# Optimization experiments

Measured on AMD Instinct MI355X. Metric: run time of the kernel, lower is better.

## Reference

```python
import jax, jax.numpy as jnp
import numpy as np
from functools import partial

N, C, D, H, W = 2, 64, 8, 96, 96
G, K, PAD = 2, 3, 1
P = K ** 3
CG = C // G
AXIS_SCALE = jnp.array([0.5, 1.0, 1.0], dtype=jnp.float32)  # applied to (dx, dy, dz)
OFFSET_SCALE = 1.0  # converged warmup scale
EPS = 1e-5


def setup_inputs() -> dict:
    key = jax.random.key(0)
    ks = jax.random.split(key, 13)
    s = 0.05
    return {
        "x": jax.random.normal(ks[0], (N, C, D, H, W), jnp.float32),
        "w_pre": jax.random.normal(ks[1], (C, C), jnp.float32) * s,
        "w_in": jax.random.normal(ks[2], (C, C), jnp.float32) * s,
        "b_in": jnp.zeros((C,), jnp.float32),
        "w_dw": jax.random.normal(ks[3], (C, 1, K, K, K), jnp.float32) * s,
        "w_off": jax.random.normal(ks[4], (C, G * P * 3), jnp.float32) * s,
        "b_off": jnp.zeros((G * P * 3,), jnp.float32),
        "w_mask": jax.random.normal(ks[5], (C, G * P), jnp.float32) * s,
        "b_mask": jnp.zeros((G * P,), jnp.float32),
        "w_out": jax.random.normal(ks[6], (C, C), jnp.float32) * s,
        "b_out": jnp.zeros((C,), jnp.float32),
        "w_post": jax.random.normal(ks[7], (C, C), jnp.float32) * s,
        "gate": jnp.zeros((), jnp.float32),
    }


def _instance_norm(x):  # x: [N, C, D, H, W], normalize over spatial dims per (n, c)
    mean = jnp.mean(x, axis=(2, 3, 4), keepdims=True)
    var = jnp.var(x, axis=(2, 3, 4), keepdims=True)
    return (x - mean) * jax.lax.rsqrt(var + EPS)


def _dcn_core(x_proj, offset, mask):
    # x_proj: [N, D, H, W, C]; offset: [N, D, H, W, G, P, 3] (dx, dy, dz); mask: [N, D, H, W, G, P]
    Dp, Hp, Wp = D + 2 * PAD, H + 2 * PAD, W + 2 * PAD
    x_pad = jnp.pad(x_proj, ((0, 0), (PAD, PAD), (PAD, PAD), (PAD, PAD), (0, 0)))
    x_pad = x_pad.reshape(N, Dp, Hp, Wp, G, CG)

    n_idx = jnp.arange(N).reshape(N, 1, 1, 1, 1)
    g_idx = jnp.arange(G).reshape(1, 1, 1, 1, G)
    zg = jnp.arange(D, dtype=jnp.float32).reshape(1, D, 1, 1, 1)
    yg = jnp.arange(H, dtype=jnp.float32).reshape(1, 1, H, 1, 1)
    xg = jnp.arange(W, dtype=jnp.float32).reshape(1, 1, 1, W, 1)

    def trilinear(zs, ys, xs):  # each [N, D, H, W, G] float coords in padded frame
        z0 = jnp.floor(zs); y0 = jnp.floor(ys); x0 = jnp.floor(xs)
        fz = zs - z0; fy = ys - y0; fx = xs - x0
        z0i = z0.astype(jnp.int32); y0i = y0.astype(jnp.int32); x0i = x0.astype(jnp.int32)
        res = None
        for dz in (0, 1):
            wz = fz if dz else 1.0 - fz
            zi = z0i + dz
            for dy in (0, 1):
                wy = fy if dy else 1.0 - fy
                yi = y0i + dy
                for dx in (0, 1):
                    wx = fx if dx else 1.0 - fx
                    xi = x0i + dx
                    valid = ((zi >= 0) & (zi < Dp) & (yi >= 0) & (yi < Hp)
                             & (xi >= 0) & (xi < Wp)).astype(zs.dtype)
                    g = x_pad[n_idx, jnp.clip(zi, 0, Dp - 1), jnp.clip(yi, 0, Hp - 1),
                              jnp.clip(xi, 0, Wp - 1), g_idx]  # [N,D,H,W,G,CG]
                    term = g * (wz * wy * wx * valid)[..., None]
                    res = term if res is None else res + term
        return res

    # kernel grid points (z-major), base position in padded frame is out_idx + k_idx
    kk = jnp.arange(K, dtype=jnp.float32)
    kz, ky, kx = jnp.meshgrid(kk, kk, kk, indexing="ij")
    kpts = jnp.stack([kz.ravel(), ky.ravel(), kx.ravel()], axis=-1)  # [P, 3]

    off = offset * (AXIS_SCALE * OFFSET_SCALE)  # scale (dx, dy, dz)
    off_p = jnp.moveaxis(off, 5, 0)    # [P, N, D, H, W, G, 3]
    mask_p = jnp.moveaxis(mask, 5, 0)  # [P, N, D, H, W, G]

    def body(acc, inp):
        o, m, kp = inp
        zs = zg + kp[0] + o[..., 2]
        ys = yg + kp[1] + o[..., 1]
        xs = xg + kp[2] + o[..., 0]
        samp = trilinear(zs, ys, xs)  # [N,D,H,W,G,CG]
        return acc + m[..., None] * samp, None

    acc0 = jnp.zeros((N, D, H, W, G, CG), x_proj.dtype)
    acc, _ = jax.lax.scan(body, acc0, (off_p, mask_p, kpts))
    return acc.reshape(N, D, H, W, C)


def _forward(x, w_pre, w_in, b_in, w_dw, w_off, b_off, w_mask, b_mask, w_out, b_out, w_post, gate):
    pre = jnp.einsum("ncdhw,oc->nodhw", x, w_pre)  # 1x1x1 conv, no bias
    x_cl = jnp.transpose(pre, (0, 2, 3, 4, 1))     # [N,D,H,W,C]
    x_proj = x_cl @ w_in + b_in
    # depthwise 3x3x3 conv + InstanceNorm + GELU for the offset/mask branch
    dw = jax.lax.conv_general_dilated(
        pre, w_dw, window_strides=(1, 1, 1), padding=((PAD, PAD),) * 3,
        feature_group_count=C, dimension_numbers=("NCDHW", "OIDHW", "NCDHW"))
    dw = jax.nn.gelu(_instance_norm(dw))
    feat = jnp.transpose(dw, (0, 2, 3, 4, 1))      # [N,D,H,W,C]
    offset = (feat @ w_off + b_off).reshape(N, D, H, W, G, P, 3)
    mask = jax.nn.softmax((feat @ w_mask + b_mask).reshape(N, D, H, W, G, P), axis=-1)
    core = _dcn_core(x_proj, offset, mask)         # [N,D,H,W,C]
    out = core @ w_out + b_out
    y = jnp.transpose(out, (0, 4, 1, 2, 3))        # back to NCDHW
    y = jnp.einsum("ncdhw,oc->nodhw", y, w_post)   # post 1x1x1 conv
    return x + jax.nn.sigmoid(gate) * y


def reference(x, w_pre, w_in, b_in, w_dw, w_off, b_off, w_mask, b_mask, w_out, b_out, w_post, gate):
    return _forward(x, w_pre, w_in, b_in, w_dw, w_off, b_off, w_mask, b_mask, w_out, b_out, w_post, gate)
```

## Files before the change

### kernel.cpp

```cpp
#include <hip/hip_runtime.h>
#include <math.h>

#define N_ 2
#define C_ 64
#define D_ 8
#define H_ 96
#define W_ 96
#define S_ (D_*H_*W_)
#define HW_ (H_*W_)
#define ZP_ 12
#define YP_ 100
#define XP_ 100
#define NSTR_ (ZP_*YP_*XP_*64)
#define ZS_ (YP_*XP_*64)
#define YS_ (XP_*64)

__device__ __forceinline__ float gelu_fast(float x) {
    float a = 0.7978845608028654f * (x + 0.044715f*x*x*x);
    float E = __expf(2.f*a);
    return x - x * __builtin_amdgcn_rcpf(E + 1.f);
}

__device__ __forceinline__ unsigned short f2bf(float f) {
    unsigned u = __float_as_uint(f);
    unsigned r = (u + 0x7fffu + ((u >> 16) & 1u)) >> 16;
    return (unsigned short)r;
}

__global__ __launch_bounds__(64) void k_prep(const float* __restrict__ w_out,
        const float* __restrict__ b_out, const float* __restrict__ w_post,
        const float* __restrict__ w_off, const float* __restrict__ b_off,
        const float* __restrict__ w_mask, const float* __restrict__ b_mask,
        float* __restrict__ W2, float* __restrict__ B2,
        float4* __restrict__ woffT4, float4* __restrict__ b4f) {
    int b = blockIdx.x;
    int t = threadIdx.x;
    float acc = 0.f;
    for (int c = 0; c < 64; ++c)
        acc = fmaf(w_out[b*64+c], w_post[t*64+c], acc);
    W2[b*64 + t] = acc;
    if (b == 0) {
        float a2 = 0.f;
        for (int c = 0; c < 64; ++c)
            a2 = fmaf(w_post[t*64+c], b_out[c], a2);
        B2[t] = a2;
    }
    if (t < 54) {
        int c = b, u = t;
        woffT4[c*64 + u] = make_float4(w_off[c*162 + u*3] * 0.5f,
                                       w_off[c*162 + u*3 + 1],
                                       w_off[c*162 + u*3 + 2],
                                       w_mask[c*54 + u]);
        if (b == 1)
            b4f[u] = make_float4(b_off[u*3] * 0.5f, b_off[u*3+1], b_off[u*3+2],
                                 b_mask[u]);
    }
}

__global__ __launch_bounds__(256) void k_pre_proj(const float* __restrict__ x,
        const float* __restrict__ w_pre, const float* __restrict__ w_in,
        const float* __restrict__ b_in, float* __restrict__ pre,
        unsigned short* __restrict__ xprojP) {
    __shared__ float lx[64][65];
    __shared__ float lwa[64][65];
    __shared__ float lwb[64][65];
    int b = blockIdx.x;
    int n = b / 1152;
    int s0 = (b % 1152) * 64;
    int tid = threadIdx.x;
    for (int idx = tid; idx < 1024; idx += 256) {
        int r = idx >> 4, q4 = (idx & 15) * 4;
        float4 vx = *(const float4*)&x[((size_t)(n*C_ + r))*S_ + s0 + q4];
        lx[r][q4] = vx.x; lx[r][q4+1] = vx.y; lx[r][q4+2] = vx.z; lx[r][q4+3] = vx.w;
        float4 va = *(const float4*)&w_pre[r*64 + q4];
        lwa[r][q4] = va.x; lwa[r][q4+1] = va.y; lwa[r][q4+2] = va.z; lwa[r][q4+3] = va.w;
        float4 vb = *(const float4*)&w_in[r*64 + q4];
        lwb[r][q4] = vb.x; lwb[r][q4+1] = vb.y; lwb[r][q4+2] = vb.z; lwb[r][q4+3] = vb.w;
    }
    __syncthreads();
    int o0 = (tid & 15) * 4;
    int v0 = (tid >> 4) * 4;
    float acc[4][4] = {};
    #pragma unroll 8
    for (int c = 0; c < 64; ++c) {
        float xv[4], wv[4];
        #pragma unroll
        for (int j = 0; j < 4; ++j) { xv[j] = lx[c][v0+j]; wv[j] = lwa[o0+j][c]; }
        #pragma unroll
        for (int vj = 0; vj < 4; ++vj)
            #pragma unroll
            for (int oj = 0; oj < 4; ++oj)
                acc[vj][oj] = fmaf(xv[vj], wv[oj], acc[vj][oj]);
    }
    #pragma unroll
    for (int vj = 0; vj < 4; ++vj) {
        float4 r = make_float4(acc[vj][0], acc[vj][1], acc[vj][2], acc[vj][3]);
        *(float4*)&pre[((size_t)(n*S_ + s0 + v0 + vj))*64 + o0] = r;
    }
    __syncthreads();
    #pragma unroll
    for (int vj = 0; vj < 4; ++vj)
        #pragma unroll
        for (int oj = 0; oj < 4; ++oj)
            lx[v0+vj][o0+oj] = acc[vj][oj];
    __syncthreads();
    float acc2[4][4];
    #pragma unroll
    for (int oj = 0; oj < 4; ++oj) {
        float bo = b_in[o0+oj];
        #pragma unroll
        for (int vj = 0; vj < 4; ++vj) acc2[vj][oj] = bo;
    }
    #pragma unroll 8
    for (int c = 0; c < 64; ++c) {
        float fv[4], wv[4];
        #pragma unroll
        for (int j = 0; j < 4; ++j) { fv[j] = lx[v0+j][c]; wv[j] = lwb[c][o0+j]; }
        #pragma unroll
        for (int vj = 0; vj < 4; ++vj)
            #pragma unroll
            for (int oj = 0; oj < 4; ++oj)
                acc2[vj][oj] = fmaf(fv[vj], wv[oj], acc2[vj][oj]);
    }
    #pragma unroll
    for (int vj = 0; vj < 4; ++vj) {
        int vox = s0 + v0 + vj;
        int z = vox / HW_;
        int rem = vox - z*HW_;
        int y = rem / W_;
        int xq = rem - y*W_;
        size_t pw = (size_t)n*NSTR_ + (size_t)(z+2)*ZS_ + (y+2)*YS_ + (xq+2)*64 + o0;
        ushort4 pk;
        pk.x = f2bf(acc2[vj][0]); pk.y = f2bf(acc2[vj][1]);
        pk.z = f2bf(acc2[vj][2]); pk.w = f2bf(acc2[vj][3]);
        *(ushort4*)&xprojP[pw] = pk;
    }
}

__global__ __launch_bounds__(256) void k_dw_stats(const float* __restrict__ pre,
        const float* __restrict__ w_dw, float* __restrict__ dw,
        float* __restrict__ psum, float* __restrict__ pss) {
    __shared__ float4 lwd[27][16];
    __shared__ float4 lsum[16][16];
    __shared__ float4 lssum[16][16];
    int b = blockIdx.x;
    int y = b % H_;
    int z = (b / H_) % D_;
    int n = b / (D_*H_);
    int tid = threadIdx.x;
    if (tid < 27*16) {
        int k = tid >> 4, c4 = tid & 15;
        lwd[k][c4] = make_float4(w_dw[(c4*4+0)*27 + k], w_dw[(c4*4+1)*27 + k],
                                 w_dw[(c4*4+2)*27 + k], w_dw[(c4*4+3)*27 + k]);
    }
    __syncthreads();
    int c4 = tid & 15, xg = tid >> 4;
    const float* preN = pre + (size_t)n*S_*64;
    float4 s4 = make_float4(0,0,0,0), ss4 = make_float4(0,0,0,0);
    for (int xx = 0; xx < 6; ++xx) {
        int xi = xg + xx*16;
        float4 acc = make_float4(0,0,0,0);
        #pragma unroll
        for (int dz = 0; dz < 3; ++dz) {
            int zz = z + dz - 1;
            if (zz < 0 || zz >= D_) continue;
            #pragma unroll
            for (int dy = 0; dy < 3; ++dy) {
                int yy = y + dy - 1;
                if (yy < 0 || yy >= H_) continue;
                int rowb = (zz*HW_ + yy*W_)*64 + c4*4;
                #pragma unroll
                for (int dx = 0; dx < 3; ++dx) {
                    int xn = xi + dx - 1;
                    if ((unsigned)xn < (unsigned)W_) {
                        float4 v = *(const float4*)&preN[rowb + (xn<<6)];
                        float4 w = lwd[dz*9+dy*3+dx][c4];
                        acc.x = fmaf(v.x, w.x, acc.x);
                        acc.y = fmaf(v.y, w.y, acc.y);
                        acc.z = fmaf(v.z, w.z, acc.z);
                        acc.w = fmaf(v.w, w.w, acc.w);
                    }
                }
            }
        }
        *(float4*)&dw[((size_t)n*S_ + z*HW_ + y*W_ + xi)*64 + c4*4] = acc;
        s4.x += acc.x; s4.y += acc.y; s4.z += acc.z; s4.w += acc.w;
        ss4.x = fmaf(acc.x, acc.x, ss4.x); ss4.y = fmaf(acc.y, acc.y, ss4.y);
        ss4.z = fmaf(acc.z, acc.z, ss4.z); ss4.w = fmaf(acc.w, acc.w, ss4.w);
    }
    lsum[xg][c4] = s4; lssum[xg][c4] = ss4;
    __syncthreads();
    if (tid < 64) {
        float s = 0.f, ss = 0.f;
        #pragma unroll
        for (int k = 0; k < 16; ++k) {
            s  += ((const float*)&lsum [k][tid>>2])[tid&3];
            ss += ((const float*)&lssum[k][tid>>2])[tid&3];
        }
        psum[tid*1536 + b] = s;
        pss [tid*1536 + b] = ss;
    }
}

__global__ void k_stats2(const float* __restrict__ psum, const float* __restrict__ pss,
                         float* __restrict__ stats) {
    int u = blockIdx.x;
    int n = u >> 6, c = u & 63;
    int l = threadIdx.x;
    float s = 0.f, ss = 0.f;
    #pragma unroll
    for (int k = 0; k < 12; ++k) {
        int row = n*768 + k*64 + l;
        s  += psum[c*1536 + row];
        ss += pss [c*1536 + row];
    }
    #pragma unroll
    for (int o2 = 32; o2 >= 1; o2 >>= 1) {
        s  += __shfl_xor(s, o2);
        ss += __shfl_xor(ss, o2);
    }
    if (l == 0) {
        float inv = 1.f / (float)S_;
        float mean = s * inv;
        float var = ss * inv - mean*mean;
        stats[n*128 + c] = mean;
        stats[n*128 + 64 + c] = rsqrtf(var + 1e-5f);
    }
}

__global__ __launch_bounds__(256) void k_dcn(const unsigned short* __restrict__ xprojP,
        const float* __restrict__ dw, const float* __restrict__ stats,
        const float4* __restrict__ woffT4, const float4* __restrict__ b4f,
        float* __restrict__ core) {
    __shared__ float featT[64][36];
    __shared__ float4 offs4[64][29];
    int tid = threadIdx.x;
    int orig = blockIdx.x;
    int bid = (orig & 7) * 576 + (orig >> 3);
    int x8 = bid % 12;
    int t1 = bid / 12;
    int y4 = t1 % 24;
    int t2 = t1 / 24;
    int z  = t2 & 7;
    int n  = t2 >> 3;
    int yb = y4*4, xb = x8*8;
    size_t voxBase = (size_t)n*S_ + (size_t)z*HW_ + yb*W_ + xb;

    {
        int c4 = (tid & 15) * 4;
        int vp = tid >> 4;
        #pragma unroll
        for (int j = 0; j < 2; ++j) {
            int vloc = vp*2 + j;
            size_t vox = voxBase + (vloc>>3)*W_ + (vloc & 7);
            float4 v = *(const float4*)&dw[vox*64 + c4];
            float vals[4] = {v.x, v.y, v.z, v.w};
            #pragma unroll
            for (int jj = 0; jj < 4; ++jj) {
                int c = c4 + jj;
                float t = (vals[jj] - stats[n*128+c]) * stats[n*128+64+c];
                featT[c][vloc] = gelu_fast(t);
            }
        }
    }
    __syncthreads();

    if (tid < 216) {
        int q = tid / 54;
        int u = tid - q*54;
        int g = u / 27, p = u - g*27;
        float4 bb = b4f[u];
        float4 aa[8];
        #pragma unroll
        for (int j = 0; j < 8; ++j) aa[j] = bb;
        for (int c = 0; c < 64; ++c) {
            float4 w = woffT4[c*64 + u];
            float4 f0 = *(const float4*)&featT[c][q*8];
            float4 f1 = *(const float4*)&featT[c][q*8 + 4];
            float ff[8] = {f0.x, f0.y, f0.z, f0.w, f1.x, f1.y, f1.z, f1.w};
            #pragma unroll
            for (int j = 0; j < 8; ++j) {
                aa[j].x = fmaf(ff[j], w.x, aa[j].x);
                aa[j].y = fmaf(ff[j], w.y, aa[j].y);
                aa[j].z = fmaf(ff[j], w.z, aa[j].z);
                aa[j].w = fmaf(ff[j], w.w, aa[j].w);
            }
        }
        #pragma unroll
        for (int j = 0; j < 8; ++j)
            offs4[(q*8+j)*2 + g][p] = aa[j];
    }
    __syncthreads();

    if (tid < 64) {
        float mx = -1e30f;
        #pragma unroll
        for (int p = 0; p < 27; ++p) mx = fmaxf(mx, offs4[tid][p].w);
        float e[27]; float ssum = 0.f;
        #pragma unroll
        for (int p = 0; p < 27; ++p) { e[p] = __expf(offs4[tid][p].w - mx); ssum += e[p]; }
        float inv = __builtin_amdgcn_rcpf(ssum);
        #pragma unroll
        for (int p = 0; p < 27; ++p) offs4[tid][p].w = e[p]*inv;
    }
    __syncthreads();

    int pair = tid >> 2;
    int vloc = pair >> 1, g = pair & 1;
    int yy = vloc >> 3, xx = vloc & 7;
    int yv = yb + yy, xv = xb + xx;
    int ch4 = (tid & 3) * 8;
    const unsigned short* __restrict__ base = xprojP + (size_t)n*NSTR_;
    int Kc = 2*ZS_ + 2*YS_ + 128 + g*32 + ch4;
    float fzb = (float)(z-1), fyb = (float)(yv-1), fxb = (float)(xv-1);
    float a0=0.f,a1=0.f,a2=0.f,a3=0.f,a4=0.f,a5=0.f,a6=0.f,a7=0.f;
    #pragma unroll
    for (int p = 0; p < 27; ++p) {
        float4 tp = offs4[pair][p];
        float zf = fzb + (float)(p/9) + tp.z;
        float yf = fyb + (float)((p/3)%3) + tp.y;
        float xf = fxb + (float)(p%3) + tp.x;
        zf = fminf(fmaxf(zf, -1.5f), (float)D_ + 0.5f);
        yf = fminf(fmaxf(yf, -1.5f), (float)H_ + 0.5f);
        xf = fminf(fmaxf(xf, -1.5f), (float)W_ + 0.5f);
        float z0f = floorf(zf), y0f = floorf(yf), x0f = floorf(xf);
        float fz = zf - z0f, fy = yf - y0f, fx = xf - x0f;
        int zi = (int)z0f, yi = (int)y0f, xi = (int)x0f;
        float wz1 = fz * tp.w, wz0 = tp.w - wz1;
        float wy1 = fy, wy0 = 1.f - fy;
        float wx1 = fx, wx0 = 1.f - fx;
        float w00 = wz0*wy0, w01 = wz0*wy1, w10 = wz1*wy0, w11 = wz1*wy1;
        float c000 = w00*wx0, c001 = w00*wx1, c010 = w01*wx0, c011 = w01*wx1;
        float c100 = w10*wx0, c101 = w10*wx1, c110 = w11*wx0, c111 = w11*wx1;
        int cw = zi*ZS_ + yi*YS_ + (xi << 6) + Kc;
        const unsigned short* p00 = base + cw;
        const unsigned short* p01 = p00 + YS_;
        const unsigned short* p10 = p00 + ZS_;
        const unsigned short* p11 = p10 + YS_;
        uint4 q000 = *(const uint4*)p00;
        uint4 q001 = *(const uint4*)(p00 + 64);
        uint4 q010 = *(const uint4*)p01;
        uint4 q011 = *(const uint4*)(p01 + 64);
        uint4 q100 = *(const uint4*)p10;
        uint4 q101 = *(const uint4*)(p10 + 64);
        uint4 q110 = *(const uint4*)p11;
        uint4 q111 = *(const uint4*)(p11 + 64);
        #define ACC8(Q, WGT) { \
            float wq = (WGT); \
            a0 = fmaf(wq, __uint_as_float((Q).x << 16), a0); \
            a1 = fmaf(wq, __uint_as_float((Q).x & 0xffff0000u), a1); \
            a2 = fmaf(wq, __uint_as_float((Q).y << 16), a2); \
            a3 = fmaf(wq, __uint_as_float((Q).y & 0xffff0000u), a3); \
            a4 = fmaf(wq, __uint_as_float((Q).z << 16), a4); \
            a5 = fmaf(wq, __uint_as_float((Q).z & 0xffff0000u), a5); \
            a6 = fmaf(wq, __uint_as_float((Q).w << 16), a6); \
            a7 = fmaf(wq, __uint_as_float((Q).w & 0xffff0000u), a7); \
        }
        ACC8(q000, c000); ACC8(q001, c001); ACC8(q010, c010); ACC8(q011, c011);
        ACC8(q100, c100); ACC8(q101, c101); ACC8(q110, c110); ACC8(q111, c111);
        #undef ACC8
    }
    size_t voxOut = voxBase + yy*W_ + xx;
    size_t ob = voxOut*64 + g*32 + ch4;
    *(float4*)&core[ob]     = make_float4(a0, a1, a2, a3);
    *(float4*)&core[ob + 4] = make_float4(a4, a5, a6, a7);
}

__global__ __launch_bounds__(256) void k_final(const float* __restrict__ core,
        const float* __restrict__ W2, const float* __restrict__ B2,
        const float* __restrict__ x, const float* __restrict__ gate,
        float* __restrict__ out) {
    __shared__ float lc[64][65];
    __shared__ float lw[64][65];
    int b = blockIdx.x;
    int n = b / 1152;
    int s0 = (b % 1152) * 64;
    int tid = threadIdx.x;
    for (int idx = tid; idx < 1024; idx += 256) {
        int r = idx >> 4, q4 = (idx & 15) * 4;
        float4 vc = *(const float4*)&core[((size_t)(n*S_ + s0 + r))*64 + q4];
        lc[r][q4] = vc.x; lc[r][q4+1] = vc.y; lc[r][q4+2] = vc.z; lc[r][q4+3] = vc.w;
        float4 vw = *(const float4*)&W2[r*64 + q4];
        lw[r][q4] = vw.x; lw[r][q4+1] = vw.y; lw[r][q4+2] = vw.z; lw[r][q4+3] = vw.w;
    }
    __syncthreads();
    float sg = 1.f / (1.f + expf(-gate[0]));
    int o0 = (tid & 15) * 4;
    int v0 = (tid >> 4) * 4;
    float acc[4][4];
    #pragma unroll
    for (int oj = 0; oj < 4; ++oj) {
        float bo = B2[o0+oj];
        #pragma unroll
        for (int vj = 0; vj < 4; ++vj) acc[vj][oj] = bo;
    }
    #pragma unroll 8
    for (int c = 0; c < 64; ++c) {
        float fv[4], wv[4];
        #pragma unroll
        for (int j = 0; j < 4; ++j) { fv[j] = lc[v0+j][c]; wv[j] = lw[c][o0+j]; }
        #pragma unroll
        for (int vj = 0; vj < 4; ++vj)
            #pragma unroll
            for (int oj = 0; oj < 4; ++oj)
                acc[vj][oj] = fmaf(fv[vj], wv[oj], acc[vj][oj]);
    }
    #pragma unroll
    for (int oj = 0; oj < 4; ++oj) {
        size_t gi = ((size_t)(n*64 + o0 + oj))*S_ + s0 + v0;
        float4 xv = *(const float4*)&x[gi];
        float4 r;
        r.x = fmaf(sg, acc[0][oj], xv.x);
        r.y = fmaf(sg, acc[1][oj], xv.y);
        r.z = fmaf(sg, acc[2][oj], xv.z);
        r.w = fmaf(sg, acc[3][oj], xv.w);
        *(float4*)&out[gi] = r;
    }
}

extern "C" void kernel_launch(void* const* d_in, const int* in_sizes, int n_in,
                              void* d_out, int out_size, void* d_ws, size_t ws_size,
                              hipStream_t stream) {
    const float* x      = (const float*)d_in[0];
    const float* w_pre  = (const float*)d_in[1];
    const float* w_in   = (const float*)d_in[2];
    const float* b_in   = (const float*)d_in[3];
    const float* w_dw   = (const float*)d_in[4];
    const float* w_off  = (const float*)d_in[5];
    const float* b_off  = (const float*)d_in[6];
    const float* w_mask = (const float*)d_in[7];
    const float* b_mask = (const float*)d_in[8];
    const float* w_out  = (const float*)d_in[9];
    const float* b_out  = (const float*)d_in[10];
    const float* w_post = (const float*)d_in[11];
    const float* gate   = (const float*)d_in[12];
    float* out = (float*)d_out;

    float* ws      = (float*)d_ws;
    unsigned short* xprojP = (unsigned short*)ws;
    float* preCore = ws + (size_t)7680000;
    float* psum    = preCore + (size_t)9437184;
    float* pss     = psum + 98304;
    float* stats   = pss + 98304;
    float* W2      = stats + 256;
    float* B2      = W2 + 4096;
    float4* woffT4 = (float4*)(B2 + 128);
    float4* b4f    = woffT4 + 4096;
    float* dwb     = out;

    hipMemsetAsync(xprojP, 0, (size_t)15360000*sizeof(unsigned short), stream);
    hipLaunchKernelGGL(k_prep,     dim3(64),   dim3(64),  0, stream,
                       w_out, b_out, w_post, w_off, b_off, w_mask, b_mask,
                       W2, B2, woffT4, b4f);
    hipLaunchKernelGGL(k_pre_proj, dim3(2304), dim3(256), 0, stream,
                       x, w_pre, w_in, b_in, preCore, xprojP);
    hipLaunchKernelGGL(k_dw_stats, dim3(1536), dim3(256), 0, stream,
                       preCore, w_dw, dwb, psum, pss);
    hipLaunchKernelGGL(k_stats2,   dim3(128),  dim3(64),  0, stream, psum, pss, stats);
    hipLaunchKernelGGL(k_dcn,      dim3(4608), dim3(256), 0, stream,
                       xprojP, dwb, stats, woffT4, b4f, preCore);
    hipLaunchKernelGGL(k_final,    dim3(2304), dim3(256), 0, stream,
                       preCore, W2, B2, x, gate, out);
}
```

Measured before the change: 340.8 us.

## Precompute DCN sampling coords once per block and store core output as bf16

Bilinear corner weights and gather base offsets are now computed once per (voxel, group, point) in a cooperative shared-memory pass, instead of being recomputed by each of the four channel-slice threads. The weights are packed as bf16 pairs and the offsets are stored in a shared union that reuses the feature buffer. The DCN output tensor is written as bf16 rather than fp32, halving the intermediate write and the read in the final kernel. Costs are an extra barrier, bf16 rounding of the interpolation weights and the core values, and a small error from reading the high bf16 half without masking off the low bits.

Result: faster. 329.4 us (-3.3%).

```diff
diff --git a/kernel.cpp b/kernel.cpp
--- a/kernel.cpp
+++ b/kernel.cpp
@@ -25,6 +25,10 @@
     unsigned u = __float_as_uint(f);
     unsigned r = (u + 0x7fffu + ((u >> 16) & 1u)) >> 16;
     return (unsigned short)r;
+}
+
+__device__ __forceinline__ unsigned pkhi(float a, float b) {
+    return __builtin_amdgcn_perm(__float_as_uint(a), __float_as_uint(b), 0x07060302u);
 }
 
 __global__ __launch_bounds__(64) void k_prep(const float* __restrict__ w_out,
@@ -231,8 +235,11 @@
 __global__ __launch_bounds__(256) void k_dcn(const unsigned short* __restrict__ xprojP,
         const float* __restrict__ dw, const float* __restrict__ stats,
         const float4* __restrict__ woffT4, const float4* __restrict__ b4f,
-        float* __restrict__ core) {
-    __shared__ float featT[64][36];
+        unsigned short* __restrict__ coreB) {
+    __shared__ union {
+        float featT[64][36];
+        int   cwl[64][27];
+    } uS;
     __shared__ float4 offs4[64][29];
     int tid = threadIdx.x;
     int orig = blockIdx.x;
@@ -259,7 +266,7 @@
             for (int jj = 0; jj < 4; ++jj) {
                 int c = c4 + jj;
                 float t = (vals[jj] - stats[n*128+c]) * stats[n*128+64+c];
-                featT[c][vloc] = gelu_fast(t);
+                uS.featT[c][vloc] = gelu_fast(t);
             }
         }
     }
@@ -275,8 +282,8 @@
         for (int j = 0; j < 8; ++j) aa[j] = bb;
         for (int c = 0; c < 64; ++c) {
             float4 w = woffT4[c*64 + u];
-            float4 f0 = *(const float4*)&featT[c][q*8];
-            float4 f1 = *(const float4*)&featT[c][q*8 + 4];
+            float4 f0 = *(const float4*)&uS.featT[c][q*8];
+            float4 f1 = *(const float4*)&uS.featT[c][q*8 + 4];
             float ff[8] = {f0.x, f0.y, f0.z, f0.w, f1.x, f1.y, f1.z, f1.w};
             #pragma unroll
             for (int j = 0; j < 8; ++j) {
@@ -305,34 +312,52 @@
     }
     __syncthreads();
 
+    {
+        int zm1 = z - 1;
+        #pragma unroll
+        for (int k = 0; k < 7; ++k) {
+            int idx = tid + k*256;
+            if (idx < 1728) {
+                int pair = idx / 27;
+                int p = idx - pair*27;
+                float4 tp = offs4[pair][p];
+                int vloc = pair >> 1, g = pair & 1;
+                int yy = vloc >> 3, xx = vloc & 7;
+                float zf = (float)(zm1 + p/9) + tp.z;
+                float yf = (float)(yb + yy - 1 + (p/3)%3) + tp.y;
+                float xf = (float)(xb + xx - 1 + p%3) + tp.x;
+                zf = fminf(fmaxf(zf, -1.5f), (float)D_ + 0.5f);
+                yf = fminf(fmaxf(yf, -1.5f), (float)H_ + 0.5f);
+                xf = fminf(fmaxf(xf, -1.5f), (float)W_ + 0.5f);
+                float z0f = floorf(zf), y0f = floorf(yf), x0f = floorf(xf);
+                float fz = zf - z0f, fy = yf - y0f, fx = xf - x0f;
+                int zi = (int)z0f, yi = (int)y0f, xi = (int)x0f;
+                float wz1 = fz * tp.w, wz0 = tp.w - wz1;
+                float wy1 = fy, wy0 = 1.f - fy;
+                float wx1 = fx, wx0 = 1.f - fx;
+                float w00 = wz0*wy0, w01 = wz0*wy1, w10 = wz1*wy0, w11 = wz1*wy1;
+                unsigned u0 = pkhi(w00*wx1, w00*wx0);
+                unsigned u1 = pkhi(w01*wx1, w01*wx0);
+                unsigned u2 = pkhi(w10*wx1, w10*wx0);
+                unsigned u3 = pkhi(w11*wx1, w11*wx0);
+                int cw = zi*ZS_ + yi*YS_ + (xi<<6) + (2*ZS_ + 2*YS_ + 128) + g*32;
+                *(uint4*)&offs4[pair][p] = make_uint4(u0,u1,u2,u3);
+                uS.cwl[pair][p] = cw;
+            }
+        }
+    }
+    __syncthreads();
+
     int pair = tid >> 2;
     int vloc = pair >> 1, g = pair & 1;
     int yy = vloc >> 3, xx = vloc & 7;
-    int yv = yb + yy, xv = xb + xx;
     int ch4 = (tid & 3) * 8;
-    const unsigned short* __restrict__ base = xprojP + (size_t)n*NSTR_;
-    int Kc = 2*ZS_ + 2*YS_ + 128 + g*32 + ch4;
-    float fzb = (float)(z-1), fyb = (float)(yv-1), fxb = (float)(xv-1);
+    const unsigned short* __restrict__ base = xprojP + (size_t)n*NSTR_ + ch4;
     float a0=0.f,a1=0.f,a2=0.f,a3=0.f,a4=0.f,a5=0.f,a6=0.f,a7=0.f;
     #pragma unroll
     for (int p = 0; p < 27; ++p) {
-        float4 tp = offs4[pair][p];
-        float zf = fzb + (float)(p/9) + tp.z;
-        float yf = fyb + (float)((p/3)%3) + tp.y;
-        float xf = fxb + (float)(p%3) + tp.x;
-        zf = fminf(fmaxf(zf, -1.5f), (float)D_ + 0.5f);
-        yf = fminf(fmaxf(yf, -1.5f), (float)H_ + 0.5f);
-        xf = fminf(fmaxf(xf, -1.5f), (float)W_ + 0.5f);
-        float z0f = floorf(zf), y0f = floorf(yf), x0f = floorf(xf);
-        float fz = zf - z0f, fy = yf - y0f, fx = xf - x0f;
-        int zi = (int)z0f, yi = (int)y0f, xi = (int)x0f;
-        float wz1 = fz * tp.w, wz0 = tp.w - wz1;
-        float wy1 = fy, wy0 = 1.f - fy;
-        float wx1 = fx, wx0 = 1.f - fx;
-        float w00 = wz0*wy0, w01 = wz0*wy1, w10 = wz1*wy0, w11 = wz1*wy1;
-        float c000 = w00*wx0, c001 = w00*wx1, c010 = w01*wx0, c011 = w01*wx1;
-        float c100 = w10*wx0, c101 = w10*wx1, c110 = w11*wx0, c111 = w11*wx1;
-        int cw = zi*ZS_ + yi*YS_ + (xi << 6) + Kc;
+        uint4 dsc = *(const uint4*)&offs4[pair][p];
+        int cw = uS.cwl[pair][p];
         const unsigned short* p00 = base + cw;
         const unsigned short* p01 = p00 + YS_;
         const unsigned short* p10 = p00 + ZS_;
@@ -345,28 +370,34 @@
         uint4 q101 = *(const uint4*)(p10 + 64);
         uint4 q110 = *(const uint4*)p11;
         uint4 q111 = *(const uint4*)(p11 + 64);
+        float c000 = __uint_as_float(dsc.x << 16), c001 = __uint_as_float(dsc.x);
+        float c010 = __uint_as_float(dsc.y << 16), c011 = __uint_as_float(dsc.y);
+        float c100 = __uint_as_float(dsc.z << 16), c101 = __uint_as_float(dsc.z);
+        float c110 = __uint_as_float(dsc.w << 16), c111 = __uint_as_float(dsc.w);
         #define ACC8(Q, WGT) { \
             float wq = (WGT); \
             a0 = fmaf(wq, __uint_as_float((Q).x << 16), a0); \
-            a1 = fmaf(wq, __uint_as_float((Q).x & 0xffff0000u), a1); \
+            a1 = fmaf(wq, __uint_as_float((Q).x), a1); \
             a2 = fmaf(wq, __uint_as_float((Q).y << 16), a2); \
-            a3 = fmaf(wq, __uint_as_float((Q).y & 0xffff0000u), a3); \
+            a3 = fmaf(wq, __uint_as_float((Q).y), a3); \
             a4 = fmaf(wq, __uint_as_float((Q).z << 16), a4); \
-            a5 = fmaf(wq, __uint_as_float((Q).z & 0xffff0000u), a5); \
+            a5 = fmaf(wq, __uint_as_float((Q).z), a5); \
             a6 = fmaf(wq, __uint_as_float((Q).w << 16), a6); \
-            a7 = fmaf(wq, __uint_as_float((Q).w & 0xffff0000u), a7); \
+            a7 = fmaf(wq, __uint_as_float((Q).w), a7); \
         }
         ACC8(q000, c000); ACC8(q001, c001); ACC8(q010, c010); ACC8(q011, c011);
         ACC8(q100, c100); ACC8(q101, c101); ACC8(q110, c110); ACC8(q111, c111);
         #undef ACC8
     }
     size_t voxOut = voxBase + yy*W_ + xx;
-    size_t ob = voxOut*64 + g*32 + ch4;
-    *(float4*)&core[ob]     = make_float4(a0, a1, a2, a3);
-    *(float4*)&core[ob + 4] = make_float4(a4, a5, a6, a7);
-}
-
-__global__ __launch_bounds__(256) void k_final(const float* __restrict__ core,
+    unsigned r01 = pkhi(a1, a0);
+    unsigned r23 = pkhi(a3, a2);
+    unsigned r45 = pkhi(a5, a4);
+    unsigned r67 = pkhi(a7, a6);
+    *(uint4*)&coreB[voxOut*64 + g*32 + ch4] = make_uint4(r01, r23, r45, r67);
+}
+
+__global__ __launch_bounds__(256) void k_final(const unsigned short* __restrict__ coreB,
         const float* __restrict__ W2, const float* __restrict__ B2,
         const float* __restrict__ x, const float* __restrict__ gate,
         float* __restrict__ out) {
@@ -376,10 +407,20 @@
     int n = b / 1152;
     int s0 = (b % 1152) * 64;
     int tid = threadIdx.x;
+    for (int idx = tid; idx < 512; idx += 256) {
+        int r = idx >> 3, q8 = (idx & 7) * 8;
+        uint4 q = *(const uint4*)&coreB[((size_t)(n*S_ + s0 + r))*64 + q8];
+        lc[r][q8+0] = __uint_as_float(q.x << 16);
+        lc[r][q8+1] = __uint_as_float(q.x & 0xffff0000u);
+        lc[r][q8+2] = __uint_as_float(q.y << 16);
+        lc[r][q8+3] = __uint_as_float(q.y & 0xffff0000u);
+        lc[r][q8+4] = __uint_as_float(q.z << 16);
+        lc[r][q8+5] = __uint_as_float(q.z & 0xffff0000u);
+        lc[r][q8+6] = __uint_as_float(q.w << 16);
+        lc[r][q8+7] = __uint_as_float(q.w & 0xffff0000u);
+    }
     for (int idx = tid; idx < 1024; idx += 256) {
         int r = idx >> 4, q4 = (idx & 15) * 4;
-        float4 vc = *(const float4*)&core[((size_t)(n*S_ + s0 + r))*64 + q4];
-        lc[r][q4] = vc.x; lc[r][q4+1] = vc.y; lc[r][q4+2] = vc.z; lc[r][q4+3] = vc.w;
         float4 vw = *(const float4*)&W2[r*64 + q4];
         lw[r][q4] = vw.x; lw[r][q4+1] = vw.y; lw[r][q4+2] = vw.z; lw[r][q4+3] = vw.w;
     }
@@ -438,8 +479,9 @@
 
     float* ws      = (float*)d_ws;
     unsigned short* xprojP = (unsigned short*)ws;
-    float* preCore = ws + (size_t)7680000;
-    float* psum    = preCore + (size_t)9437184;
+    float* pre     = ws + (size_t)7680000;
+    unsigned short* coreB = (unsigned short*)(pre + (size_t)9437184);
+    float* psum    = (float*)(coreB + (size_t)9437184);
     float* pss     = psum + 98304;
     float* stats   = pss + 98304;
     float* W2      = stats + 256;
@@ -453,12 +495,12 @@
                        w_out, b_out, w_post, w_off, b_off, w_mask, b_mask,
                        W2, B2, woffT4, b4f);
     hipLaunchKernelGGL(k_pre_proj, dim3(2304), dim3(256), 0, stream,
-                       x, w_pre, w_in, b_in, preCore, xprojP);
+                       x, w_pre, w_in, b_in, pre, xprojP);
     hipLaunchKernelGGL(k_dw_stats, dim3(1536), dim3(256), 0, stream,
-                       preCore, w_dw, dwb, psum, pss);
+                       pre, w_dw, dwb, psum, pss);
     hipLaunchKernelGGL(k_stats2,   dim3(128),  dim3(64),  0, stream, psum, pss, stats);
     hipLaunchKernelGGL(k_dcn,      dim3(4608), dim3(256), 0, stream,
-                       xprojP, dwb, stats, woffT4, b4f, preCore);
+                       xprojP, dwb, stats, woffT4, b4f, coreB);
     hipLaunchKernelGGL(k_final,    dim3(2304), dim3(256), 0, stream,
-                       preCore, W2, B2, x, gate, out);
-}
+                       coreB, W2, B2, x, gate, out);
+}
```
